# Kernel tuning notes

Measured on AMD Instinct MI355X. Metric: run time of the kernel, lower is better.

The kernel has to match this reference:

```python
import jax, jax.numpy as jnp
import numpy as np

N_HEADS, D_MODEL, D_HEAD = 16, 1024, 64
EPSILON = -100000.0  # module uses -1e5, not -inf
INIT_STD = 0.02


def setup_inputs() -> dict:
    key = jax.random.key(0)
    ks = jax.random.split(key, 5)
    B, S = 4, 2048
    x = jax.random.normal(ks[0], (B, S, D_MODEL), dtype=jnp.float32)
    W_Q = INIT_STD * jax.random.normal(ks[1], (N_HEADS, D_MODEL, D_HEAD), dtype=jnp.float32)
    W_K = INIT_STD * jax.random.normal(ks[2], (N_HEADS, D_MODEL, D_HEAD), dtype=jnp.float32)
    W_V = INIT_STD * jax.random.normal(ks[3], (N_HEADS, D_MODEL, D_HEAD), dtype=jnp.float32)
    W_O = INIT_STD * jax.random.normal(ks[4], (N_HEADS, D_HEAD, D_MODEL), dtype=jnp.float32)
    b_Q = jnp.zeros((N_HEADS, D_HEAD), jnp.float32)
    b_K = jnp.zeros((N_HEADS, D_HEAD), jnp.float32)
    b_V = jnp.zeros((N_HEADS, D_HEAD), jnp.float32)
    b_O = jnp.zeros((D_MODEL,), jnp.float32)
    return {"normalized_resid_pre": x, "W_Q": W_Q, "b_Q": b_Q, "W_K": W_K,
            "b_K": b_K, "W_V": W_V, "b_V": b_V, "W_O": W_O, "b_O": b_O}


def reference(normalized_resid_pre, W_Q, b_Q, W_K, b_K, W_V, b_V, W_O, b_O):
    x = normalized_resid_pre  # [b, s, e]
    q = jnp.einsum('bse,neh->bsnh', x, W_Q) + b_Q
    k = jnp.einsum('bse,neh->bsnh', x, W_K) + b_K
    v = jnp.einsum('bse,neh->bsnh', x, W_V) + b_V
    scores = jnp.einsum('bqnh,bknh->bnqk', q, k) / jnp.sqrt(jnp.float32(D_HEAD))
    sq, sk = scores.shape[-2], scores.shape[-1]
    causal = jnp.triu(jnp.ones((sq, sk), bool), k=1)  # True above diagonal
    scores = jnp.where(causal, jnp.float32(EPSILON), scores)
    probs = jax.nn.softmax(scores, axis=-1)
    z = jnp.einsum('bnqk,bknh->bqnh', probs, v)
    # sum over heads of per-head output projection + bias
    attn_out = jnp.einsum('bqnh,nhe->bqe', z, W_O) + b_O
    return attn_out
```

## Files before the change

### kernel.cpp

```cpp
#include <hip/hip_runtime.h>


typedef __attribute__((ext_vector_type(8))) short short8;
typedef __attribute__((ext_vector_type(4))) float floatx4;

__device__ __forceinline__ float bf2f(unsigned short u) {
  union { unsigned int i; float f; } v; v.i = ((unsigned int)u) << 16; return v.f;
}
__device__ __forceinline__ unsigned short f2bf(float f) {
  unsigned int x = __float_as_uint(f);
  x += 0x7fffu + ((x >> 16) & 1u);
  return (unsigned short)(x >> 16);
}

__device__ __forceinline__ void gload_lds16(const unsigned short* g, unsigned short* lds) {
  __builtin_amdgcn_global_load_lds(
      (const __attribute__((address_space(1))) void*)g,
      (__attribute__((address_space(3))) void*)lds, 16, 0, 0);
}

__global__ __launch_bounds__(256) void cvt_x_kernel(const float* __restrict__ X,
                                                    unsigned short* __restrict__ Xb) {
  int idx = (blockIdx.x << 8) + threadIdx.x;
  Xb[idx] = f2bf(X[idx]);
}

__global__ __launch_bounds__(256) void transpose_wqkv3(const float* __restrict__ Wq,
                                                       const float* __restrict__ Wk,
                                                       const float* __restrict__ Wv,
                                                       unsigned short* __restrict__ Bt) {
  int idx = (blockIdx.x << 8) + threadIdx.x;
  int c = idx >> 10, e = idx & 1023;
  int proj = c >> 10, cc = c & 1023;
  int nn = cc >> 6, h = cc & 63;
  const float* W = (proj == 0) ? Wq : (proj == 1) ? Wk : Wv;
  Bt[idx] = f2bf(W[((size_t)nn << 16) + (e << 6) + h]);
}

__global__ __launch_bounds__(256) void transpose_wo(const float* __restrict__ W,
                                                    unsigned short* __restrict__ Wt) {
  int idx = (blockIdx.x << 8) + threadIdx.x;
  int e = idx >> 10, k = idx & 1023;
  Wt[idx] = f2bf(W[((size_t)k << 10) + e]);
}

template <int MODE>
__global__ __launch_bounds__(256) void gemm128_kernel(
    const unsigned short* __restrict__ A,
    const unsigned short* __restrict__ Bt,
    const float* __restrict__ b0, const float* __restrict__ b1,
    const float* __restrict__ b2,
    unsigned short* __restrict__ Oq, unsigned short* __restrict__ Ok,
    unsigned short* __restrict__ Ov, float* __restrict__ Of)
{
  const int K = 1024;
  __shared__ __align__(16) unsigned short As[4096];
  __shared__ __align__(16) unsigned short Bs[4096];
  const int tid = threadIdx.x;
  const int l   = tid & 63, w = tid >> 6;
  const int l15 = l & 15,  lg = l >> 4;
  const int mo  = (w >> 1) << 6, no = (w & 1) << 6;
  const int m0  = blockIdx.y << 7, n0 = blockIdx.x << 7;
  const int lrow = l >> 2;
  const int lcol = (l & 3) << 3;

  floatx4 acc[4][4];
#pragma unroll
  for (int i = 0; i < 4; ++i)
#pragma unroll
    for (int j = 0; j < 4; ++j) acc[i][j] = (floatx4){0.f, 0.f, 0.f, 0.f};

  for (int k0 = 0; k0 < K; k0 += 32) {
    __syncthreads();
#pragma unroll
    for (int j = 0; j < 2; ++j) {
      int seg = (w << 1) + j;
      int row = (seg << 4) + lrow;
      gload_lds16(A  + (size_t)(m0 + row) * K + k0 + lcol, &As[seg << 9]);
      gload_lds16(Bt + (size_t)(n0 + row) * K + k0 + lcol, &Bs[seg << 9]);
    }
    __syncthreads();
    short8 af[4], bf[4];
#pragma unroll
    for (int mc = 0; mc < 4; ++mc)
      af[mc] = *(const short8*)&As[((mo + (mc << 4) + l15) << 5) + (lg << 3)];
#pragma unroll
    for (int nc = 0; nc < 4; ++nc)
      bf[nc] = *(const short8*)&Bs[((no + (nc << 4) + l15) << 5) + (lg << 3)];
#pragma unroll
    for (int mc = 0; mc < 4; ++mc)
#pragma unroll
      for (int nc = 0; nc < 4; ++nc)
        acc[mc][nc] = __builtin_amdgcn_mfma_f32_16x16x32_bf16(af[mc], bf[nc], acc[mc][nc], 0, 0, 0);
  }

#pragma unroll
  for (int nc = 0; nc < 4; ++nc) {
    int c = n0 + no + (nc << 4) + l15;
    if (MODE == 1) {
      float bv = b0[c];
#pragma unroll
      for (int mc = 0; mc < 4; ++mc)
#pragma unroll
        for (int r = 0; r < 4; ++r) {
          int m = m0 + mo + (mc << 4) + (lg << 2) + r;
          Of[((size_t)m << 10) + c] = acc[mc][nc][r] + bv;
        }
    } else {
      int proj = c >> 10, cc = c & 1023;
      int hn = cc >> 6, h = cc & 63;
      const float* bp = (proj == 0) ? b0 : (proj == 1) ? b1 : b2;
      float bv = bp[cc];
      if (proj < 2) {
        unsigned short* O = (proj == 0) ? Oq : Ok;
#pragma unroll
        for (int mc = 0; mc < 4; ++mc)
#pragma unroll
          for (int r = 0; r < 4; ++r) {
            int m = m0 + mo + (mc << 4) + (lg << 2) + r;
            int bb = m >> 11, ss = m & 2047;
            O[((((size_t)(bb << 4) + hn) << 11) + ss) * 64 + h] = f2bf(acc[mc][nc][r] + bv);
          }
      } else {
#pragma unroll
        for (int mc = 0; mc < 4; ++mc) {
          int m = m0 + mo + (mc << 4) + (lg << 2);
          int bb = m >> 11, ss = m & 2047;
          unsigned short p0 = f2bf(acc[mc][nc][0] + bv);
          unsigned short p1 = f2bf(acc[mc][nc][1] + bv);
          unsigned short p2 = f2bf(acc[mc][nc][2] + bv);
          unsigned short p3 = f2bf(acc[mc][nc][3] + bv);
          uint2 pk;
          pk.x = (unsigned int)p0 | ((unsigned int)p1 << 16);
          pk.y = (unsigned int)p2 | ((unsigned int)p3 << 16);
          *(uint2*)&Ov[((((size_t)(bb << 4) + hn) << 6) + h) * 2048 + ss] = pk;
        }
      }
    }
  }
}

#define FSTR 72
#define SCL 0.1803368801111244f

__global__ __launch_bounds__(256) void flash2_kernel(
    const unsigned short* __restrict__ Q,
    const unsigned short* __restrict__ K,
    const unsigned short* __restrict__ Vt,
    unsigned short* __restrict__ Z)
{
  __shared__ __align__(16) unsigned short Ks[64 * FSTR];
  __shared__ __align__(16) unsigned short Vs[64 * FSTR];
  __shared__ __align__(16) unsigned short Ps[4][32 * FSTR];

  const int tid = threadIdx.x;
  const int l   = tid & 63, w = tid >> 6;
  const int l15 = l & 15,  lg = l >> 4;
  const int n = blockIdx.y, b = blockIdx.z;
  const size_t hoff = (size_t)((b << 4) + n) << 17;
  const unsigned short* Qh = Q + hoff;
  const unsigned short* Kh = K + hoff;
  const unsigned short* Vh = Vt + hoff;

  const int srow = tid >> 2;
  const int scol = (tid & 3) << 4;

  short8 onef;
#pragma unroll
  for (int i = 0; i < 8; ++i) onef[i] = (short)0x3F80;

  for (int half = 0; half < 2; ++half) {
    const int qt  = half ? (15 - (int)blockIdx.x) : (int)blockIdx.x;
    const int q0w = (qt << 7) + (w << 5);

    short8 qf[2][2];
#pragma unroll
    for (int qc = 0; qc < 2; ++qc)
#pragma unroll
      for (int dh = 0; dh < 2; ++dh)
        qf[qc][dh] = *(const short8*)(Qh + (size_t)(q0w + (qc << 4) + l15) * 64 + (dh << 5) + (lg << 3));

    floatx4 acc_o[2][4], acc_l[2];
#pragma unroll
    for (int qc = 0; qc < 2; ++qc) {
      acc_l[qc] = (floatx4){0.f, 0.f, 0.f, 0.f};
#pragma unroll
      for (int dc = 0; dc < 4; ++dc) acc_o[qc][dc] = (floatx4){0.f, 0.f, 0.f, 0.f};
    }

    const int nkt = (qt << 1) + 2;
    for (int kt = 0; kt < nkt; ++kt) {
      const int k0 = kt << 6;
      __syncthreads();
      *(int4*)&Ks[srow * FSTR + scol]     = *(const int4*)(Kh + (size_t)(k0 + srow) * 64 + scol);
      *(int4*)&Ks[srow * FSTR + scol + 8] = *(const int4*)(Kh + (size_t)(k0 + srow) * 64 + scol + 8);
      *(int4*)&Vs[srow * FSTR + scol]     = *(const int4*)(Vh + (size_t)srow * 2048 + k0 + scol);
      *(int4*)&Vs[srow * FSTR + scol + 8] = *(const int4*)(Vh + (size_t)srow * 2048 + k0 + scol + 8);
      __syncthreads();
      if (k0 > q0w + 31) continue;

      floatx4 s[2][4];
#pragma unroll
      for (int qc = 0; qc < 2; ++qc)
#pragma unroll
        for (int mc = 0; mc < 4; ++mc) s[qc][mc] = (floatx4){0.f, 0.f, 0.f, 0.f};
#pragma unroll
      for (int dh = 0; dh < 2; ++dh)
#pragma unroll
        for (int mc = 0; mc < 4; ++mc) {
          short8 ak = *(const short8*)&Ks[((mc << 4) + l15) * FSTR + (dh << 5) + (lg << 3)];
          s[0][mc] = __builtin_amdgcn_mfma_f32_16x16x32_bf16(ak, qf[0][dh], s[0][mc], 0, 0, 0);
          s[1][mc] = __builtin_amdgcn_mfma_f32_16x16x32_bf16(ak, qf[1][dh], s[1][mc], 0, 0, 0);
        }

#pragma unroll
      for (int qc = 0; qc < 2; ++qc) {
        int qg = q0w + (qc << 4) + l15;
#pragma unroll
        for (int mc = 0; mc < 4; ++mc) {
          unsigned short pp[4];
#pragma unroll
          for (int r = 0; r < 4; ++r) {
            int key = k0 + (mc << 4) + (lg << 2) + r;
            float p = (key > qg) ? 0.f : exp2f(s[qc][mc][r] * SCL);
            pp[r] = f2bf(p);
          }
          uint2 pk;
          pk.x = (unsigned int)pp[0] | ((unsigned int)pp[1] << 16);
          pk.y = (unsigned int)pp[2] | ((unsigned int)pp[3] << 16);
          *(uint2*)&Ps[w][((qc << 4) + l15) * FSTR + (mc << 4) + (lg << 2)] = pk;
        }
      }

      short8 pa[2][2];
#pragma unroll
      for (int qc = 0; qc < 2; ++qc)
#pragma unroll
        for (int kc = 0; kc < 2; ++kc)
          pa[qc][kc] = *(const short8*)&Ps[w][((qc << 4) + l15) * FSTR + (kc << 5) + (lg << 3)];
#pragma unroll
      for (int dc = 0; dc < 4; ++dc)
#pragma unroll
        for (int kc = 0; kc < 2; ++kc) {
          short8 vb = *(const short8*)&Vs[((dc << 4) + l15) * FSTR + (kc << 5) + (lg << 3)];
          acc_o[0][dc] = __builtin_amdgcn_mfma_f32_16x16x32_bf16(pa[0][kc], vb, acc_o[0][dc], 0, 0, 0);
          acc_o[1][dc] = __builtin_amdgcn_mfma_f32_16x16x32_bf16(pa[1][kc], vb, acc_o[1][dc], 0, 0, 0);
        }
#pragma unroll
      for (int qc = 0; qc < 2; ++qc)
#pragma unroll
        for (int kc = 0; kc < 2; ++kc)
          acc_l[qc] = __builtin_amdgcn_mfma_f32_16x16x32_bf16(pa[qc][kc], onef, acc_l[qc], 0, 0, 0);
    }

#pragma unroll
    for (int qc = 0; qc < 2; ++qc) {
      floatx4 inv;
#pragma unroll
      for (int r = 0; r < 4; ++r) inv[r] = 1.f / acc_l[qc][r];
#pragma unroll
      for (int dc = 0; dc < 4; ++dc)
#pragma unroll
        for (int r = 0; r < 4; ++r) {
          int qg = q0w + (qc << 4) + (lg << 2) + r;
          Z[(((size_t)b << 11) + qg) * 1024 + (n << 6) + (dc << 4) + l15] =
              f2bf(acc_o[qc][dc][r] * inv[r]);
        }
    }
  }
}

extern "C" void kernel_launch(void* const* d_in, const int* in_sizes, int n_in,
                              void* d_out, int out_size, void* d_ws, size_t ws_size,
                              hipStream_t stream) {
  const float* x   = (const float*)d_in[0];
  const float* W_Q = (const float*)d_in[1];
  const float* b_Q = (const float*)d_in[2];
  const float* W_K = (const float*)d_in[3];
  const float* b_K = (const float*)d_in[4];
  const float* W_V = (const float*)d_in[5];
  const float* b_V = (const float*)d_in[6];
  const float* W_O = (const float*)d_in[7];
  const float* b_O = (const float*)d_in[8];
  float* out = (float*)d_out;

  unsigned short* ws    = (unsigned short*)d_ws;
  unsigned short* BtQKV = ws;
  unsigned short* Wo_t  = BtQKV + (3u << 20);
  unsigned short* Xb    = Wo_t + (1u << 20);
  unsigned short* Qb    = Xb + (8u << 20);
  unsigned short* Kb    = Qb + (8u << 20);
  unsigned short* Vtb   = Kb + (8u << 20);
  unsigned short* Zb    = Vtb + (8u << 20);

  cvt_x_kernel   <<<32768, 256, 0, stream>>>(x, Xb);
  transpose_wqkv3<<<12288, 256, 0, stream>>>(W_Q, W_K, W_V, BtQKV);
  transpose_wo   <<<4096, 256, 0, stream>>>(W_O, Wo_t);

  gemm128_kernel<0><<<dim3(24, 64), 256, 0, stream>>>(
      Xb, BtQKV, b_Q, b_K, b_V, Qb, Kb, Vtb, nullptr);

  flash2_kernel<<<dim3(8, 16, 4), 256, 0, stream>>>(Qb, Kb, Vtb, Zb);

  gemm128_kernel<1><<<dim3(8, 64), 256, 0, stream>>>(
      Zb, Wo_t, b_O, nullptr, nullptr, nullptr, nullptr, nullptr, out);
}
```

Measured before the change: 324.2 us.

## Vectorize conversions, tile weight transposes, and rework flash kernel loads and scaling

The x conversion kernel now uses float4 loads. The weight transposes go through LDS tiles so reads and writes are coalesced. The softmax scale is folded into Q in the QKV GEMM epilogue. The flash kernel loads K/V with direct global-to-LDS loads into an XOR-swizzled layout, applies the causal mask only on diagonal tiles, and packs P by truncation instead of round-to-nearest. It also remaps blocks to a 1D grid that groups heads, and caps launch bounds at 2 blocks per CU. The truncated bf16 P and the scale folded before Q rounding add small numerical differences.

```diff
diff --git a/kernel.cpp b/kernel.cpp
--- a/kernel.cpp
+++ b/kernel.cpp
@@ -4,9 +4,8 @@
 typedef __attribute__((ext_vector_type(8))) short short8;
 typedef __attribute__((ext_vector_type(4))) float floatx4;
 
-__device__ __forceinline__ float bf2f(unsigned short u) {
-  union { unsigned int i; float f; } v; v.i = ((unsigned int)u) << 16; return v.f;
-}
+#define SCL 0.1803368801111244f
+
 __device__ __forceinline__ unsigned short f2bf(float f) {
   unsigned int x = __float_as_uint(f);
   x += 0x7fffu + ((x >> 16) & 1u);
@@ -21,27 +20,67 @@
 
 __global__ __launch_bounds__(256) void cvt_x_kernel(const float* __restrict__ X,
                                                     unsigned short* __restrict__ Xb) {
-  int idx = (blockIdx.x << 8) + threadIdx.x;
-  Xb[idx] = f2bf(X[idx]);
-}
-
-__global__ __launch_bounds__(256) void transpose_wqkv3(const float* __restrict__ Wq,
-                                                       const float* __restrict__ Wk,
-                                                       const float* __restrict__ Wv,
-                                                       unsigned short* __restrict__ Bt) {
-  int idx = (blockIdx.x << 8) + threadIdx.x;
-  int c = idx >> 10, e = idx & 1023;
-  int proj = c >> 10, cc = c & 1023;
-  int nn = cc >> 6, h = cc & 63;
+  int idx = ((blockIdx.x << 8) + threadIdx.x) << 2;
+  float4 f = *(const float4*)(X + idx);
+  unsigned short u[4] = { f2bf(f.x), f2bf(f.y), f2bf(f.z), f2bf(f.w) };
+  *(uint2*)(Xb + idx) = *(uint2*)u;
+}
+
+__global__ __launch_bounds__(256) void transpose_wqkv3(
+    const float* __restrict__ Wq, const float* __restrict__ Wk,
+    const float* __restrict__ Wv, unsigned short* __restrict__ Bt) {
+  __shared__ unsigned short T[64 * 72];
+  const int t = threadIdx.x;
+  const int e0 = blockIdx.x << 6, nn = blockIdx.y, proj = blockIdx.z;
   const float* W = (proj == 0) ? Wq : (proj == 1) ? Wk : Wv;
-  Bt[idx] = f2bf(W[((size_t)nn << 16) + (e << 6) + h]);
+  const float* src = W + ((size_t)nn << 16) + ((size_t)e0 << 6);
+#pragma unroll
+  for (int rnd = 0; rnd < 4; ++rnd) {
+    int off = (rnd << 10) + (t << 2);
+    float4 f = *(const float4*)(src + off);
+    int r = off >> 6, h = off & 63;
+    T[r * 72 + h]     = f2bf(f.x);
+    T[r * 72 + h + 1] = f2bf(f.y);
+    T[r * 72 + h + 2] = f2bf(f.z);
+    T[r * 72 + h + 3] = f2bf(f.w);
+  }
+  __syncthreads();
+  const int h = t >> 2, ck = t & 3;
+  size_t orow = ((size_t)((proj << 10) + (nn << 6) + h) << 10) + e0 + (ck << 4);
+#pragma unroll
+  for (int g = 0; g < 2; ++g) {
+    unsigned short v[8];
+#pragma unroll
+    for (int j = 0; j < 8; ++j) v[j] = T[((ck << 4) + (g << 3) + j) * 72 + h];
+    *(int4*)(Bt + orow + (g << 3)) = *(int4*)v;
+  }
 }
 
 __global__ __launch_bounds__(256) void transpose_wo(const float* __restrict__ W,
                                                     unsigned short* __restrict__ Wt) {
-  int idx = (blockIdx.x << 8) + threadIdx.x;
-  int e = idx >> 10, k = idx & 1023;
-  Wt[idx] = f2bf(W[((size_t)k << 10) + e]);
+  __shared__ unsigned short T[64 * 72];
+  const int t = threadIdx.x;
+  const int e0 = blockIdx.x << 6, k0 = blockIdx.y << 6;
+#pragma unroll
+  for (int rnd = 0; rnd < 4; ++rnd) {
+    int r = (rnd << 4) + (t >> 4);
+    int c = (t & 15) << 2;
+    float4 f = *(const float4*)(W + ((size_t)(k0 + r) << 10) + e0 + c);
+    T[r * 72 + c]     = f2bf(f.x);
+    T[r * 72 + c + 1] = f2bf(f.y);
+    T[r * 72 + c + 2] = f2bf(f.z);
+    T[r * 72 + c + 3] = f2bf(f.w);
+  }
+  __syncthreads();
+  const int i = t >> 2, ck = t & 3;
+  size_t orow = ((size_t)(e0 + i) << 10) + k0 + (ck << 4);
+#pragma unroll
+  for (int g = 0; g < 2; ++g) {
+    unsigned short v[8];
+#pragma unroll
+    for (int j = 0; j < 8; ++j) v[j] = T[((ck << 4) + (g << 3) + j) * 72 + i];
+    *(int4*)(Wt + orow + (g << 3)) = *(int4*)v;
+  }
 }
 
 template <int MODE>
@@ -111,6 +150,7 @@
       int hn = cc >> 6, h = cc & 63;
       const float* bp = (proj == 0) ? b0 : (proj == 1) ? b1 : b2;
       float bv = bp[cc];
+      float sc = (proj == 0) ? SCL : 1.0f;
       if (proj < 2) {
         unsigned short* O = (proj == 0) ? Oq : Ok;
 #pragma unroll
@@ -119,7 +159,7 @@
           for (int r = 0; r < 4; ++r) {
             int m = m0 + mo + (mc << 4) + (lg << 2) + r;
             int bb = m >> 11, ss = m & 2047;
-            O[((((size_t)(bb << 4) + hn) << 11) + ss) * 64 + h] = f2bf(acc[mc][nc][r] + bv);
+            O[((((size_t)(bb << 4) + hn) << 11) + ss) * 64 + h] = f2bf((acc[mc][nc][r] + bv) * sc);
           }
       } else {
 #pragma unroll
@@ -140,37 +180,41 @@
   }
 }
 
-#define FSTR 72
-#define SCL 0.1803368801111244f
-
-__global__ __launch_bounds__(256) void flash2_kernel(
+__global__ __launch_bounds__(256, 2) void flash3_kernel(
     const unsigned short* __restrict__ Q,
     const unsigned short* __restrict__ K,
     const unsigned short* __restrict__ Vt,
     unsigned short* __restrict__ Z)
 {
-  __shared__ __align__(16) unsigned short Ks[64 * FSTR];
-  __shared__ __align__(16) unsigned short Vs[64 * FSTR];
-  __shared__ __align__(16) unsigned short Ps[4][32 * FSTR];
+  __shared__ __align__(16) unsigned short Ks[4096];
+  __shared__ __align__(16) unsigned short Vs[4096];
+  __shared__ __align__(16) unsigned short Ps[4 * 2304];
 
   const int tid = threadIdx.x;
   const int l   = tid & 63, w = tid >> 6;
   const int l15 = l & 15,  lg = l >> 4;
-  const int n = blockIdx.y, b = blockIdx.z;
-  const size_t hoff = (size_t)((b << 4) + n) << 17;
+  const int x    = blockIdx.x;
+  const int head = ((x & 7) << 3) + ((x >> 6) & 7);
+  const int pairidx = (x >> 3) & 7;
+  const int n = head & 15, b = head >> 4;
+  const size_t hoff = (size_t)head << 17;
   const unsigned short* Qh = Q + hoff;
   const unsigned short* Kh = K + hoff;
   const unsigned short* Vh = Vt + hoff;
-
-  const int srow = tid >> 2;
-  const int scol = (tid & 3) << 4;
+  unsigned short* Psw = Ps + w * 2304;
+
+  const int srow8 = l >> 3;
+  const int sblk8 = ((l & 7) ^ srow8) << 3;
+  const int swz   = l15 & 7;
+  const int bo0   = (lg ^ swz) << 3;
+  const int bo1   = ((4 + lg) ^ swz) << 3;
 
   short8 onef;
 #pragma unroll
   for (int i = 0; i < 8; ++i) onef[i] = (short)0x3F80;
 
   for (int half = 0; half < 2; ++half) {
-    const int qt  = half ? (15 - (int)blockIdx.x) : (int)blockIdx.x;
+    const int qt  = half ? (15 - pairidx) : pairidx;
     const int q0w = (qt << 7) + (w << 5);
 
     short8 qf[2][2];
@@ -192,43 +236,52 @@
     for (int kt = 0; kt < nkt; ++kt) {
       const int k0 = kt << 6;
       __syncthreads();
-      *(int4*)&Ks[srow * FSTR + scol]     = *(const int4*)(Kh + (size_t)(k0 + srow) * 64 + scol);
-      *(int4*)&Ks[srow * FSTR + scol + 8] = *(const int4*)(Kh + (size_t)(k0 + srow) * 64 + scol + 8);
-      *(int4*)&Vs[srow * FSTR + scol]     = *(const int4*)(Vh + (size_t)srow * 2048 + k0 + scol);
-      *(int4*)&Vs[srow * FSTR + scol + 8] = *(const int4*)(Vh + (size_t)srow * 2048 + k0 + scol + 8);
+#pragma unroll
+      for (int j = 0; j < 2; ++j) {
+        const int s = (w << 1) + j;
+        gload_lds16(Kh + (size_t)(k0 + (s << 3) + srow8) * 64 + sblk8, &Ks[s << 9]);
+        gload_lds16(Vh + (size_t)((s << 3) + srow8) * 2048 + k0 + sblk8, &Vs[s << 9]);
+      }
       __syncthreads();
       if (k0 > q0w + 31) continue;
 
-      floatx4 s[2][4];
-#pragma unroll
-      for (int qc = 0; qc < 2; ++qc)
-#pragma unroll
-        for (int mc = 0; mc < 4; ++mc) s[qc][mc] = (floatx4){0.f, 0.f, 0.f, 0.f};
-#pragma unroll
-      for (int dh = 0; dh < 2; ++dh)
+      floatx4 s0[4], s1[4];
+#pragma unroll
+      for (int mc = 0; mc < 4; ++mc) {
+        s0[mc] = (floatx4){0.f, 0.f, 0.f, 0.f};
+        s1[mc] = (floatx4){0.f, 0.f, 0.f, 0.f};
+      }
+#pragma unroll
+      for (int dh = 0; dh < 2; ++dh) {
+        const int bo = dh ? bo1 : bo0;
 #pragma unroll
         for (int mc = 0; mc < 4; ++mc) {
-          short8 ak = *(const short8*)&Ks[((mc << 4) + l15) * FSTR + (dh << 5) + (lg << 3)];
-          s[0][mc] = __builtin_amdgcn_mfma_f32_16x16x32_bf16(ak, qf[0][dh], s[0][mc], 0, 0, 0);
-          s[1][mc] = __builtin_amdgcn_mfma_f32_16x16x32_bf16(ak, qf[1][dh], s[1][mc], 0, 0, 0);
-        }
-
+          short8 ak = *(const short8*)&Ks[(((mc << 4) + l15) << 6) + bo];
+          s0[mc] = __builtin_amdgcn_mfma_f32_16x16x32_bf16(ak, qf[0][dh], s0[mc], 0, 0, 0);
+          s1[mc] = __builtin_amdgcn_mfma_f32_16x16x32_bf16(ak, qf[1][dh], s1[mc], 0, 0, 0);
+        }
+      }
+
+      const bool needmask = (k0 + 63 > q0w);
 #pragma unroll
       for (int qc = 0; qc < 2; ++qc) {
-        int qg = q0w + (qc << 4) + l15;
+        const int qg = q0w + (qc << 4) + l15;
 #pragma unroll
         for (int mc = 0; mc < 4; ++mc) {
-          unsigned short pp[4];
+          float p[4];
 #pragma unroll
           for (int r = 0; r < 4; ++r) {
-            int key = k0 + (mc << 4) + (lg << 2) + r;
-            float p = (key > qg) ? 0.f : exp2f(s[qc][mc][r] * SCL);
-            pp[r] = f2bf(p);
+            float e = exp2f(qc ? s1[mc][r] : s0[mc][r]);
+            if (needmask) {
+              int key = k0 + (mc << 4) + (lg << 2) + r;
+              e = (key > qg) ? 0.f : e;
+            }
+            p[r] = e;
           }
           uint2 pk;
-          pk.x = (unsigned int)pp[0] | ((unsigned int)pp[1] << 16);
-          pk.y = (unsigned int)pp[2] | ((unsigned int)pp[3] << 16);
-          *(uint2*)&Ps[w][((qc << 4) + l15) * FSTR + (mc << 4) + (lg << 2)] = pk;
+          pk.x = (__float_as_uint(p[1]) & 0xFFFF0000u) | (__float_as_uint(p[0]) >> 16);
+          pk.y = (__float_as_uint(p[3]) & 0xFFFF0000u) | (__float_as_uint(p[2]) >> 16);
+          *(uint2*)&Psw[((qc << 4) + l15) * 72 + (mc << 4) + (lg << 2)] = pk;
         }
       }
 
@@ -237,20 +290,19 @@
       for (int qc = 0; qc < 2; ++qc)
 #pragma unroll
         for (int kc = 0; kc < 2; ++kc)
-          pa[qc][kc] = *(const short8*)&Ps[w][((qc << 4) + l15) * FSTR + (kc << 5) + (lg << 3)];
-#pragma unroll
-      for (int dc = 0; dc < 4; ++dc)
-#pragma unroll
-        for (int kc = 0; kc < 2; ++kc) {
-          short8 vb = *(const short8*)&Vs[((dc << 4) + l15) * FSTR + (kc << 5) + (lg << 3)];
+          pa[qc][kc] = *(const short8*)&Psw[((qc << 4) + l15) * 72 + (kc << 5) + (lg << 3)];
+#pragma unroll
+      for (int kc = 0; kc < 2; ++kc) {
+        const int bo = kc ? bo1 : bo0;
+#pragma unroll
+        for (int dc = 0; dc < 4; ++dc) {
+          short8 vb = *(const short8*)&Vs[(((dc << 4) + l15) << 6) + bo];
           acc_o[0][dc] = __builtin_amdgcn_mfma_f32_16x16x32_bf16(pa[0][kc], vb, acc_o[0][dc], 0, 0, 0);
           acc_o[1][dc] = __builtin_amdgcn_mfma_f32_16x16x32_bf16(pa[1][kc], vb, acc_o[1][dc], 0, 0, 0);
         }
-#pragma unroll
-      for (int qc = 0; qc < 2; ++qc)
-#pragma unroll
-        for (int kc = 0; kc < 2; ++kc)
-          acc_l[qc] = __builtin_amdgcn_mfma_f32_16x16x32_bf16(pa[qc][kc], onef, acc_l[qc], 0, 0, 0);
+        acc_l[0] = __builtin_amdgcn_mfma_f32_16x16x32_bf16(pa[0][kc], onef, acc_l[0], 0, 0, 0);
+        acc_l[1] = __builtin_amdgcn_mfma_f32_16x16x32_bf16(pa[1][kc], onef, acc_l[1], 0, 0, 0);
+      }
     }
 
 #pragma unroll
@@ -293,14 +345,14 @@
   unsigned short* Vtb   = Kb + (8u << 20);
   unsigned short* Zb    = Vtb + (8u << 20);
 
-  cvt_x_kernel   <<<32768, 256, 0, stream>>>(x, Xb);
-  transpose_wqkv3<<<12288, 256, 0, stream>>>(W_Q, W_K, W_V, BtQKV);
-  transpose_wo   <<<4096, 256, 0, stream>>>(W_O, Wo_t);
+  cvt_x_kernel   <<<8192, 256, 0, stream>>>(x, Xb);
+  transpose_wqkv3<<<dim3(16, 16, 3), 256, 0, stream>>>(W_Q, W_K, W_V, BtQKV);
+  transpose_wo   <<<dim3(16, 16), 256, 0, stream>>>(W_O, Wo_t);
 
   gemm128_kernel<0><<<dim3(24, 64), 256, 0, stream>>>(
       Xb, BtQKV, b_Q, b_K, b_V, Qb, Kb, Vtb, nullptr);
 
-  flash2_kernel<<<dim3(8, 16, 4), 256, 0, stream>>>(Qb, Kb, Vtb, Zb);
+  flash3_kernel<<<512, 256, 0, stream>>>(Qb, Kb, Vtb, Zb);
 
   gemm128_kernel<1><<<dim3(8, 64), 256, 0, stream>>>(
       Zb, Wo_t, b_O, nullptr, nullptr, nullptr, nullptr, nullptr, out);
```

New measurement: 285.3 us. -12.0%, faster.
